# Kernel optimization log

Hardware: AMD Instinct MI355X
Metric: run time of the kernel (lower is better)

## Reference

```python
import jax, jax.numpy as jnp
import numpy as np

EMBED_DIM = 768
NUM_HEADS = 12
HEAD_DIM = EMBED_DIM // NUM_HEADS
SEGMENT_LENGTHS = [2048, 4096, 8192]
DILATION_RATES = [1, 2, 4]
SCALE = 1.0 / np.sqrt(HEAD_DIM)
B, S = 1, 8192


def setup_inputs() -> dict:
    key = jax.random.key(0)
    ks = jax.random.split(key, 5)
    std = 1.0 / np.sqrt(EMBED_DIM)
    return {
        "x": jax.random.normal(ks[0], (B, S, EMBED_DIM), dtype=jnp.float32),
        "Wqkv": jax.random.normal(ks[1], (EMBED_DIM, 3 * EMBED_DIM), dtype=jnp.float32) * std,
        "bqkv": jax.random.normal(ks[2], (3 * EMBED_DIM,), dtype=jnp.float32) * 0.01,
        "Wout": jax.random.normal(ks[3], (EMBED_DIM, EMBED_DIM), dtype=jnp.float32) * std,
        "bout": jax.random.normal(ks[4], (EMBED_DIM,), dtype=jnp.float32) * 0.01,
    }


def _attend(q, k, v):
    # q,k,v: [B,H,L,D]; full softmax attention (non-causal)
    scores = jnp.einsum("bhqd,bhkd->bhqk", q, k) * SCALE
    w = jax.nn.softmax(scores, axis=-1)
    return jnp.einsum("bhqk,bhkd->bhqd", w, v)


def reference(x, Wqkv, bqkv, Wout, bout):
    b, s, _ = x.shape
    qkv = x @ Wqkv + bqkv                                  # [B,S,3E]
    qkv = qkv.reshape(b, s, 3, NUM_HEADS, HEAD_DIM)
    qkv = jnp.transpose(qkv, (2, 0, 3, 1, 4))              # [3,B,H,S,D]
    q, k, v = qkv[0], qkv[1], qkv[2]

    outputs = []
    for seg_len, dil in zip(SEGMENT_LENGTHS, DILATION_RATES):
        if seg_len > s:
            continue
        if dil > 1:
            idx = np.arange(0, s, dil)[:seg_len]           # static indices
            seg_out = _attend(q[:, :, idx, :], k[:, :, idx, :], v[:, :, idx, :])
            full = jnp.zeros((b, NUM_HEADS, s, HEAD_DIM), dtype=seg_out.dtype)
            full = full.at[:, :, idx, :].set(seg_out)
        else:
            seg_out = _attend(q[:, :, :seg_len, :], k[:, :, :seg_len, :], v[:, :, :seg_len, :])
            pad = s - seg_out.shape[2]
            full = jnp.pad(seg_out, ((0, 0), (0, 0), (0, pad), (0, 0))) if pad > 0 else seg_out
        outputs.append(full)

    out = jnp.mean(jnp.stack(outputs), axis=0) if len(outputs) > 1 else outputs[0]
    out = jnp.transpose(out, (0, 2, 1, 3)).reshape(b, s, EMBED_DIM)
    return out @ Wout + bout
```

## Files before the change

### kernel.cpp

```cpp
#include <hip/hip_runtime.h>
#include <hip/hip_bf16.h>

typedef float f32x4 __attribute__((ext_vector_type(4)));
typedef float fvec4 __attribute__((ext_vector_type(4)));
typedef __bf16 bf16x8 __attribute__((ext_vector_type(8)));
typedef __bf16 bf16x2 __attribute__((ext_vector_type(2)));

__device__ inline float fexp2(float x) {
#if __has_builtin(__builtin_amdgcn_exp2f)
    return __builtin_amdgcn_exp2f(x);
#else
    return exp2f(x);
#endif
}

__device__ __forceinline__ bf16x2 pk_bf16(float a, float b) {
#if __has_builtin(__builtin_amdgcn_cvt_pk_bf16_f32)
    auto t = __builtin_amdgcn_cvt_pk_bf16_f32(a, b);
    return __builtin_bit_cast(bf16x2, t);
#else
    bf16x2 r; r[0] = (__bf16)a; r[1] = (__bf16)b; return r;
#endif
}

#define MFMA_BF16(a, b, c) __builtin_amdgcn_mfma_f32_16x16x32_bf16((a), (b), (c), 0, 0, 0)
#define SCHED_FENCE() __builtin_amdgcn_sched_barrier(0)

__device__ __forceinline__ void gl2lds16(const void* g, void* l) {
    __builtin_amdgcn_global_load_lds((const __attribute__((address_space(1))) void*)g,
                                     (__attribute__((address_space(3))) void*)l, 16, 0, 0);
}

#define SEG1OFF ((size_t)12 * 2048 * 64)
#define SEG2OFF ((size_t)12 * 6144 * 64)
#define QSCALE 0.18033688f

__global__ __launch_bounds__(256) void prep_kernel(
    const float* __restrict__ x, const float* __restrict__ Wqkv,
    const float* __restrict__ Wout, __bf16* __restrict__ xb,
    __bf16* __restrict__ WqkvT, __bf16* __restrict__ WoutT) {
    int bid = blockIdx.x, tid = threadIdx.x;
    if (bid < 3072) {
        int i = bid * 256 + tid;
        fvec4 a = ((const fvec4*)x)[2 * i];
        fvec4 b = ((const fvec4*)x)[2 * i + 1];
        bf16x8 o;
        o[0] = (__bf16)a[0]; o[1] = (__bf16)a[1]; o[2] = (__bf16)a[2]; o[3] = (__bf16)a[3];
        o[4] = (__bf16)b[0]; o[5] = (__bf16)b[1]; o[6] = (__bf16)b[2]; o[7] = (__bf16)b[3];
        ((bf16x8*)xb)[i] = o;
    } else if (bid < 3936) {
        int b = bid - 3072;
        int n = (b % 9) * 256 + tid;
        int kg = b / 9;
        bf16x8 o;
#pragma unroll
        for (int j = 0; j < 8; j++) o[j] = (__bf16)Wqkv[(size_t)(kg * 8 + j) * 2304 + n];
        *(bf16x8*)&WqkvT[(size_t)n * 768 + kg * 8] = o;
    } else {
        int b = bid - 3936;
        int n = (b % 3) * 256 + tid;
        int kg = b / 3;
        bf16x8 o;
#pragma unroll
        for (int j = 0; j < 8; j++) o[j] = (__bf16)Wout[(size_t)(kg * 8 + j) * 768 + n];
        *(bf16x8*)&WoutT[(size_t)n * 768 + kg * 8] = o;
    }
}

__global__ __launch_bounds__(256) void vtrans_kernel(const __bf16* __restrict__ Vc,
                                                     __bf16* __restrict__ Vt) {
    __shared__ __bf16 T[64][68];
    int bid = blockIdx.x;
    int Lc, head, t;
    size_t soff;
    if (bid < 768)       { Lc = 4096; head = bid >> 6; t = bid & 63; soff = SEG1OFF; }
    else if (bid < 1152) { int i = bid - 768; Lc = 2048; head = i >> 5; t = i & 31; soff = 0; }
    else                 { int i = bid - 1152; Lc = 2048; head = i >> 5; t = i & 31; soff = SEG2OFF; }
    const __bf16* src = Vc + soff + (size_t)head * Lc * 64;
    __bf16* dst = Vt + soff + (size_t)head * 64 * Lc;
    int tid = threadIdx.x;
#pragma unroll
    for (int it = 0; it < 2; it++) {
        int s = tid + it * 256;
        int kvr = s >> 3, d8 = (s & 7) * 8;
        bf16x8 vv = *(const bf16x8*)&src[(size_t)(t * 64 + kvr) * 64 + d8];
#pragma unroll
        for (int j = 0; j < 8; j++) T[d8 + j][kvr] = vv[j];
    }
    __syncthreads();
#pragma unroll
    for (int it = 0; it < 2; it++) {
        int s = tid + it * 256;
        int d = s >> 3, ck = s & 7;
        int kb = (ck >> 2) * 32 + (ck & 3) * 4;
        bf16x8 o;
#pragma unroll
        for (int J = 0; J < 8; J++) o[J] = T[d][kb + (J & 3) + (J >> 2) * 16];
        *(bf16x8*)&dst[(size_t)d * Lc + t * 64 + ck * 8] = o;
    }
}

__global__ __launch_bounds__(256, 2) void gemm_qkv_kernel(
    const __bf16* __restrict__ Ab, const __bf16* __restrict__ Bt,
    const float* __restrict__ bias,
    __bf16* __restrict__ Qc, __bf16* __restrict__ Kc, __bf16* __restrict__ Vc) {
    __shared__ __align__(16) char smem[65536];
    __bf16* T = (__bf16*)smem;
    int tid = threadIdx.x;
    int wave = tid >> 6, lane = tid & 63;
    int quad = lane >> 4, l15 = lane & 15;
    int bm = blockIdx.x * 128, bn = blockIdx.y * 128;
    int wm = (wave >> 1) * 64, wn = (wave & 1) * 64;
    int swzA = tid & 7;
    int rows_[4], chs_[4];
#pragma unroll
    for (int j = 0; j < 4; j++) {
        int s = j * 256 + tid;
        rows_[j] = s >> 3;
        chs_[j] = swzA ^ (rows_[j] & 7);
    }
    f32x4 acc[4][4] = {};
    {
#pragma unroll
        for (int j = 0; j < 4; j++) {
            gl2lds16(&Ab[(size_t)(bm + rows_[j]) * 768 + chs_[j] * 8],
                     smem + j * 4096 + wave * 1024);
            gl2lds16(&Bt[(size_t)(bn + rows_[j]) * 768 + chs_[j] * 8],
                     smem + 16384 + j * 4096 + wave * 1024);
        }
    }
    for (int ki = 0; ki < 12; ki++) {
        __syncthreads();
        int cur = ki & 1;
        if (ki + 1 < 12) {
            int nb = (cur ^ 1) * 32768;
            int k1 = (ki + 1) * 64;
#pragma unroll
            for (int j = 0; j < 4; j++) {
                gl2lds16(&Ab[(size_t)(bm + rows_[j]) * 768 + k1 + chs_[j] * 8],
                         smem + nb + j * 4096 + wave * 1024);
                gl2lds16(&Bt[(size_t)(bn + rows_[j]) * 768 + k1 + chs_[j] * 8],
                         smem + nb + 16384 + j * 4096 + wave * 1024);
            }
        }
        const __bf16* Al = (const __bf16*)(smem + cur * 32768);
        const __bf16* Bl = Al + 8192;
#pragma unroll
        for (int ks = 0; ks < 2; ks++) {
            bf16x8 af[4], bfr[4];
#pragma unroll
            for (int i = 0; i < 4; i++) {
                int row = wm + i * 16 + l15;
                af[i] = *(const bf16x8*)&Al[row * 64 + (((ks * 4 + quad) ^ (row & 7)) * 8)];
            }
#pragma unroll
            for (int j = 0; j < 4; j++) {
                int row = wn + j * 16 + l15;
                bfr[j] = *(const bf16x8*)&Bl[row * 64 + (((ks * 4 + quad) ^ (row & 7)) * 8)];
            }
#pragma unroll
            for (int i = 0; i < 4; i++)
#pragma unroll
                for (int j = 0; j < 4; j++)
                    acc[i][j] = MFMA_BF16(af[i], bfr[j], acc[i][j]);
        }
    }
    int which = blockIdx.y / 6;
    int h0 = (blockIdx.y % 6) * 2;
    float scl = which == 0 ? QSCALE : 1.0f;
    float bv[4];
#pragma unroll
    for (int j = 0; j < 4; j++) bv[j] = bias[bn + wn + j * 16 + l15];
    __syncthreads();
#pragma unroll
    for (int i = 0; i < 4; i++)
#pragma unroll
        for (int j = 0; j < 4; j++) {
            int col = wn + j * 16 + l15;
#pragma unroll
            for (int r = 0; r < 4; r++) {
                int row = wm + i * 16 + quad * 4 + r;
                int ch = ((col >> 3) & 8) | (((col >> 3) & 7) ^ (row & 7));
                T[row * 136 + ch * 8 + (col & 7)] =
                    (__bf16)((acc[i][j][r] + bv[j]) * scl);
            }
        }
    __syncthreads();
    __bf16* dst = which == 0 ? Qc : (which == 1 ? Kc : Vc);
    int rr = tid >> 4;
    int c8 = tid & 15;
    int hh = c8 >> 3, d8 = c8 & 7;
    int h = h0 + hh;
    __bf16* p0 = dst + ((size_t)h * 2048 * 64) + d8 * 8;
    __bf16* p1 = dst + SEG1OFF + ((size_t)h * 4096 * 64) + d8 * 8;
    __bf16* p2 = dst + SEG2OFF + ((size_t)h * 2048 * 64) + d8 * 8;
#pragma unroll
    for (int pass = 0; pass < 8; pass++) {
        int row = pass * 16 + rr;
        int pos = bm + row;
        int ch = (c8 & 8) | ((c8 & 7) ^ (row & 7));
        bf16x8 v = *(const bf16x8*)&T[row * 136 + ch * 8];
        if (pos < 2048) *(bf16x8*)&p0[(size_t)pos * 64] = v;
        if (!(pos & 1)) *(bf16x8*)&p1[(size_t)(pos >> 1) * 64] = v;
        if (!(pos & 3)) *(bf16x8*)&p2[(size_t)(pos >> 2) * 64] = v;
    }
}

__global__ __launch_bounds__(256) void gemm_out_kernel(
    const __bf16* __restrict__ Ab, const __bf16* __restrict__ Bt,
    const float* __restrict__ bias, float* __restrict__ Co) {
    __shared__ __align__(16) char smem[49152];
    int tid = threadIdx.x;
    int wave = tid >> 6, lane = tid & 63;
    int quad = lane >> 4, l15 = lane & 15;
    int bm = blockIdx.x * 64, bn = blockIdx.y * 128;
    int wn = wave * 32;
    int rowsA[2], chsA[2], rowsB[4], chsB[4];
#pragma unroll
    for (int j = 0; j < 2; j++) {
        int s = j * 256 + tid;
        rowsA[j] = s >> 3;
        chsA[j] = (s & 7) ^ (rowsA[j] & 7);
    }
#pragma unroll
    for (int j = 0; j < 4; j++) {
        int s = j * 256 + tid;
        rowsB[j] = s >> 3;
        chsB[j] = (s & 7) ^ (rowsB[j] & 7);
    }
    f32x4 acc[4][2] = {};
    {
#pragma unroll
        for (int j = 0; j < 2; j++)
            gl2lds16(&Ab[(size_t)(bm + rowsA[j]) * 768 + chsA[j] * 8],
                     smem + j * 4096 + wave * 1024);
#pragma unroll
        for (int j = 0; j < 4; j++)
            gl2lds16(&Bt[(size_t)(bn + rowsB[j]) * 768 + chsB[j] * 8],
                     smem + 8192 + j * 4096 + wave * 1024);
    }
    for (int ki = 0; ki < 12; ki++) {
        __syncthreads();
        int cur = ki & 1;
        if (ki + 1 < 12) {
            int nb = (cur ^ 1) * 24576;
            int k1 = (ki + 1) * 64;
#pragma unroll
            for (int j = 0; j < 2; j++)
                gl2lds16(&Ab[(size_t)(bm + rowsA[j]) * 768 + k1 + chsA[j] * 8],
                         smem + nb + j * 4096 + wave * 1024);
#pragma unroll
            for (int j = 0; j < 4; j++)
                gl2lds16(&Bt[(size_t)(bn + rowsB[j]) * 768 + k1 + chsB[j] * 8],
                         smem + nb + 8192 + j * 4096 + wave * 1024);
        }
        const __bf16* Al = (const __bf16*)(smem + cur * 24576);
        const __bf16* Bl = Al + 4096;
#pragma unroll
        for (int ks = 0; ks < 2; ks++) {
            bf16x8 af[4], bfr[2];
#pragma unroll
            for (int i = 0; i < 4; i++) {
                int row = i * 16 + l15;
                af[i] = *(const bf16x8*)&Al[row * 64 + (((ks * 4 + quad) ^ (row & 7)) * 8)];
            }
#pragma unroll
            for (int j = 0; j < 2; j++) {
                int row = wn + j * 16 + l15;
                bfr[j] = *(const bf16x8*)&Bl[row * 64 + (((ks * 4 + quad) ^ (row & 7)) * 8)];
            }
#pragma unroll
            for (int i = 0; i < 4; i++)
#pragma unroll
                for (int j = 0; j < 2; j++)
                    acc[i][j] = MFMA_BF16(af[i], bfr[j], acc[i][j]);
        }
    }
#pragma unroll
    for (int j = 0; j < 2; j++) {
        int c = bn + wn + j * 16 + l15;
        float bv = bias[c];
#pragma unroll
        for (int i = 0; i < 4; i++)
#pragma unroll
            for (int r = 0; r < 4; r++) {
                int row = bm + i * 16 + quad * 4 + r;
                Co[(size_t)row * 768 + c] = acc[i][j][r] + bv;
            }
    }
}

__global__ __launch_bounds__(256, 2) void attn_kernel(
    const __bf16* __restrict__ Qcb, const __bf16* __restrict__ Kcb,
    const __bf16* __restrict__ Vtb,
    float* __restrict__ O0, float* __restrict__ O1a, float* __restrict__ O1b,
    float* __restrict__ O1c, float* __restrict__ O1d, float* __restrict__ O2,
    float* __restrict__ L0, float* __restrict__ L1a, float* __restrict__ L1b,
    float* __restrict__ L1c, float* __restrict__ L1d, float* __restrict__ L2) {
    __shared__ __bf16 Kl[2 * 4096];
    __shared__ __bf16 Vl[2 * 4096];
    int bid = blockIdx.x;
    int seg, piece = 0, head, qt, Lc, iters;
    if (bid < 192)      { seg = 0; head = bid >> 4; qt = bid & 15; Lc = 2048; iters = 32; }
    else if (bid < 384) { int i = bid - 192; seg = 2; head = i >> 4; qt = i & 15; Lc = 2048; iters = 32; }
    else                { int i = bid - 384; seg = 1; head = i >> 7; int r = i & 127;
                          qt = r >> 2; piece = r & 3; Lc = 4096; iters = 16; }
    size_t soff = seg == 0 ? 0 : (seg == 1 ? SEG1OFF : SEG2OFF);
    const __bf16* Qh = Qcb + soff + (size_t)head * Lc * 64;
    const __bf16* Kh = Kcb + soff + (size_t)head * Lc * 64;
    const __bf16* Vh = Vtb + soff + (size_t)head * 64 * Lc;
    float* Ob;
    float* Lb;
    if (seg == 0)      { Ob = O0; Lb = L0 + head * 2048; }
    else if (seg == 2) { Ob = O2; Lb = L2 + head * 2048; }
    else {
        Ob = piece == 0 ? O1a : (piece == 1 ? O1b : (piece == 2 ? O1c : O1d));
        Lb = (piece == 0 ? L1a : (piece == 1 ? L1b : (piece == 2 ? L1c : L1d))) + head * 4096;
    }
    int kvb = piece * 16;
    int tid = threadIdx.x, wave = tid >> 6, lane = tid & 63;
    int quad = lane >> 4, l15 = lane & 15;
    bf16x8 qf[2][2];
#pragma unroll
    for (int qg = 0; qg < 2; qg++) {
        size_t qpos = (size_t)(qt * 128 + wave * 32 + qg * 16 + l15);
        qf[qg][0] = *(const bf16x8*)&Qh[qpos * 64 + quad * 8];
        qf[qg][1] = *(const bf16x8*)&Qh[qpos * 64 + 32 + quad * 8];
    }
    f32x4 o[2][4] = {};
    f32x4 lacc[2] = {};
    bf16x8 ones;
#pragma unroll
    for (int j = 0; j < 8; j++) ones[j] = (__bf16)1.0f;
    int kv0 = tid >> 3, cl0 = tid & 7;
    int kdb0 = cl0 ^ (kv0 & 7);
    int kv1 = kv0 + 32, kdb1 = cl0 ^ (kv1 & 7);
    char* KlB = (char*)Kl;
    char* VlB = (char*)Vl;
    int swz = l15 & 7;
    {
        int t0 = kvb * 64;
        gl2lds16(&Kh[(size_t)(t0 + kv0) * 64 + kdb0 * 8], KlB + wave * 1024);
        gl2lds16(&Kh[(size_t)(t0 + kv1) * 64 + kdb1 * 8], KlB + 4096 + wave * 1024);
        SCHED_FENCE();
        gl2lds16(&Vh[(size_t)kv0 * Lc + t0 + kdb0 * 8], VlB + wave * 1024);
        gl2lds16(&Vh[(size_t)kv1 * Lc + t0 + kdb1 * 8], VlB + 4096 + wave * 1024);
    }
    for (int nt = 0; nt < iters; nt++) {
        int cur = nt & 1;
        SCHED_FENCE();
        asm volatile("s_waitcnt vmcnt(2)" ::: "memory");
        __builtin_amdgcn_s_barrier();
        SCHED_FENCE();
        if (nt + 1 < iters) {
            int nb = 8192 * (cur ^ 1);
            int t1 = (kvb + nt + 1) * 64;
            gl2lds16(&Kh[(size_t)(t1 + kv0) * 64 + kdb0 * 8], KlB + nb + wave * 1024);
            gl2lds16(&Kh[(size_t)(t1 + kv1) * 64 + kdb1 * 8], KlB + nb + 4096 + wave * 1024);
            SCHED_FENCE();
            gl2lds16(&Vh[(size_t)kv0 * Lc + t1 + kdb0 * 8], VlB + nb + wave * 1024);
            gl2lds16(&Vh[(size_t)kv1 * Lc + t1 + kdb1 * 8], VlB + nb + 4096 + wave * 1024);
        }
        SCHED_FENCE();
        const __bf16* Kt = Kl + cur * 4096;
        const __bf16* Vt_ = Vl + cur * 4096;
        f32x4 sarr[4][2];
        __builtin_amdgcn_s_setprio(1);
#pragma unroll
        for (int c = 0; c < 4; c++) {
            int krow = (c * 16 + l15) * 64;
            bf16x8 kf0 = *(const bf16x8*)&Kt[krow + ((quad ^ swz) * 8)];
            bf16x8 kf1 = *(const bf16x8*)&Kt[krow + (((4 + quad) ^ swz) * 8)];
#pragma unroll
            for (int qg = 0; qg < 2; qg++) {
                f32x4 z = {};
                z = MFMA_BF16(kf0, qf[qg][0], z);
                sarr[c][qg] = MFMA_BF16(kf1, qf[qg][1], z);
            }
        }
        __builtin_amdgcn_s_setprio(0);
        union { bf16x8 v8; bf16x2 v2[4]; } pf8[2][2];
#pragma unroll
        for (int qg = 0; qg < 2; qg++)
#pragma unroll
            for (int c = 0; c < 4; c++) {
                float p0 = fexp2(sarr[c][qg][0]);
                float p1 = fexp2(sarr[c][qg][1]);
                float p2 = fexp2(sarr[c][qg][2]);
                float p3 = fexp2(sarr[c][qg][3]);
                pf8[qg][c >> 1].v2[(c & 1) * 2 + 0] = pk_bf16(p0, p1);
                pf8[qg][c >> 1].v2[(c & 1) * 2 + 1] = pk_bf16(p2, p3);
            }
        SCHED_FENCE();
        if (nt + 1 < iters) {
            asm volatile("s_waitcnt vmcnt(4)" ::: "memory");
        } else {
            asm volatile("s_waitcnt vmcnt(0)" ::: "memory");
        }
        __builtin_amdgcn_s_barrier();
        SCHED_FENCE();
        __builtin_amdgcn_s_setprio(1);
#pragma unroll
        for (int u = 0; u < 2; u++) {
#pragma unroll
            for (int ds = 0; ds < 4; ds++) {
                int d = ds * 16 + l15;
                bf16x8 vf = *(const bf16x8*)&Vt_[d * 64 + (((u * 4 + quad) ^ swz) * 8)];
                o[0][ds] = MFMA_BF16(vf, pf8[0][u].v8, o[0][ds]);
                o[1][ds] = MFMA_BF16(vf, pf8[1][u].v8, o[1][ds]);
            }
            lacc[0] = MFMA_BF16(ones, pf8[0][u].v8, lacc[0]);
            lacc[1] = MFMA_BF16(ones, pf8[1][u].v8, lacc[1]);
        }
        __builtin_amdgcn_s_setprio(0);
    }
#pragma unroll
    for (int qg = 0; qg < 2; qg++) {
        float l = lacc[qg][0];
        int pos = qt * 128 + wave * 32 + qg * 16 + l15;
        float* orow = Ob + (size_t)pos * 768 + head * 64;
#pragma unroll
        for (int ds = 0; ds < 4; ds++)
            *(f32x4*)&orow[ds * 16 + quad * 4] = o[qg][ds];
        if (lane < 16) Lb[qt * 128 + wave * 32 + qg * 16 + lane] = l;
    }
}

__global__ __launch_bounds__(256) void combine_kernel(
    const float* __restrict__ O0, const float* __restrict__ O1a,
    const float* __restrict__ O1b, const float* __restrict__ O1c,
    const float* __restrict__ O1d, const float* __restrict__ O2,
    const float* __restrict__ L0, const float* __restrict__ L1a,
    const float* __restrict__ L1b, const float* __restrict__ L1c,
    const float* __restrict__ L1d, const float* __restrict__ L2,
    __bf16* __restrict__ attnF) {
    int g = blockIdx.x * 256 + threadIdx.x;
    int q = g / 96;
    int cs = (g - q * 96) * 8;
    int head = cs >> 6;
    f32x4 a0 = {}, a1 = {};
    if (q < 2048) {
        float inv = 1.0f / L0[head * 2048 + q];
        const f32x4* p = (const f32x4*)&O0[(size_t)q * 768 + cs];
        a0 += p[0] * inv; a1 += p[1] * inv;
    }
    if (!(q & 1)) {
        int p1 = q >> 1;
        int li = head * 4096 + p1;
        float inv = 1.0f / (L1a[li] + L1b[li] + L1c[li] + L1d[li]);
        size_t ro = (size_t)p1 * 768 + cs;
        const f32x4* pa = (const f32x4*)&O1a[ro];
        const f32x4* pb = (const f32x4*)&O1b[ro];
        const f32x4* pc = (const f32x4*)&O1c[ro];
        const f32x4* pd = (const f32x4*)&O1d[ro];
        a0 += ((pa[0] + pb[0]) + (pc[0] + pd[0])) * inv;
        a1 += ((pa[1] + pb[1]) + (pc[1] + pd[1])) * inv;
    }
    if (!(q & 3)) {
        int p2 = q >> 2;
        float inv = 1.0f / L2[head * 2048 + p2];
        const f32x4* p = (const f32x4*)&O2[(size_t)p2 * 768 + cs];
        a0 += p[0] * inv; a1 += p[1] * inv;
    }
    const float third = 1.0f / 3.0f;
    bf16x8 ov;
    ov[0] = (__bf16)(a0[0] * third); ov[1] = (__bf16)(a0[1] * third);
    ov[2] = (__bf16)(a0[2] * third); ov[3] = (__bf16)(a0[3] * third);
    ov[4] = (__bf16)(a1[0] * third); ov[5] = (__bf16)(a1[1] * third);
    ov[6] = (__bf16)(a1[2] * third); ov[7] = (__bf16)(a1[3] * third);
    *(bf16x8*)&attnF[(size_t)q * 768 + cs] = ov;
}

extern "C" void kernel_launch(void* const* d_in, const int* in_sizes, int n_in,
                              void* d_out, int out_size, void* d_ws, size_t ws_size,
                              hipStream_t stream) {
    const float* x    = (const float*)d_in[0];
    const float* Wqkv = (const float*)d_in[1];
    const float* bqkv = (const float*)d_in[2];
    const float* Wout = (const float*)d_in[3];
    const float* bout = (const float*)d_in[4];
    float* out = (float*)d_out;
    (void)in_sizes; (void)n_in; (void)out_size; (void)ws_size;

    char* ws = (char*)d_ws;
    size_t off = 0;
    auto take = [&](size_t bytes) -> void* {
        void* p = ws + off;
        off += (bytes + 255) & ~(size_t)255;
        return p;
    };
    const size_t QKV_ELEMS = (size_t)12 * 8192 * 64;
    __bf16* xb    = (__bf16*)take((size_t)8192 * 768 * 2);
    __bf16* WqkvT = (__bf16*)take((size_t)2304 * 768 * 2);
    __bf16* WoutT = (__bf16*)take((size_t)768 * 768 * 2);
    __bf16* Qc    = (__bf16*)take(QKV_ELEMS * 2);
    __bf16* Kc    = (__bf16*)take(QKV_ELEMS * 2);
    __bf16* Vc    = (__bf16*)take(QKV_ELEMS * 2);
    __bf16* Vt    = (__bf16*)take(QKV_ELEMS * 2);
    float*  O1a   = (float*)take((size_t)4096 * 768 * 4);
    float*  O1b   = (float*)take((size_t)4096 * 768 * 4);
    float*  O1c   = (float*)take((size_t)4096 * 768 * 4);
    float*  L0    = (float*)take((size_t)12 * 2048 * 4);
    float*  L1a   = (float*)take((size_t)12 * 4096 * 4);
    float*  L1b   = (float*)take((size_t)12 * 4096 * 4);
    float*  L1c   = (float*)take((size_t)12 * 4096 * 4);
    float*  L1d   = (float*)take((size_t)12 * 4096 * 4);
    float*  L2    = (float*)take((size_t)12 * 2048 * 4);
    float*  O0    = (float*)xb;
    float*  O2    = O0 + (size_t)2048 * 768;
    float*  O1d   = (float*)Vc;
    __bf16* attnF = Qc;

    prep_kernel<<<4224, 256, 0, stream>>>(x, Wqkv, Wout, xb, WqkvT, WoutT);
    gemm_qkv_kernel<<<dim3(64, 18), 256, 0, stream>>>(xb, WqkvT, bqkv, Qc, Kc, Vc);
    vtrans_kernel<<<1536, 256, 0, stream>>>(Vc, Vt);
    attn_kernel<<<1920, 256, 0, stream>>>(Qc, Kc, Vt, O0, O1a, O1b, O1c, O1d, O2,
                                          L0, L1a, L1b, L1c, L1d, L2);
    combine_kernel<<<3072, 256, 0, stream>>>(O0, O1a, O1b, O1c, O1d, O2,
                                             L0, L1a, L1b, L1c, L1d, L2, attnF);
    gemm_out_kernel<<<dim3(128, 6), 256, 0, stream>>>(attnF, WoutT, bout, out);
}
```

Measured before the change: 244.7 us.

## Fuse V transpose into QKV GEMM epilogue and reorder attention block mapping

Removes the separate V-transpose kernel. The QKV GEMM epilogue now writes V directly in transposed, permuted layout for all three dilated segments, reading from the swizzled shared-memory tile. This saves a kernel launch and a round trip of V through global memory, at the cost of strided shared-memory gathers in the epilogue. Separately, the attention kernel's block index mapping now places the head innermost, which changes the order in which blocks are scheduled and may affect cache locality.

```diff
diff --git a/kernel.cpp b/kernel.cpp
--- a/kernel.cpp
+++ b/kernel.cpp
@@ -67,43 +67,10 @@
     }
 }
 
-__global__ __launch_bounds__(256) void vtrans_kernel(const __bf16* __restrict__ Vc,
-                                                     __bf16* __restrict__ Vt) {
-    __shared__ __bf16 T[64][68];
-    int bid = blockIdx.x;
-    int Lc, head, t;
-    size_t soff;
-    if (bid < 768)       { Lc = 4096; head = bid >> 6; t = bid & 63; soff = SEG1OFF; }
-    else if (bid < 1152) { int i = bid - 768; Lc = 2048; head = i >> 5; t = i & 31; soff = 0; }
-    else                 { int i = bid - 1152; Lc = 2048; head = i >> 5; t = i & 31; soff = SEG2OFF; }
-    const __bf16* src = Vc + soff + (size_t)head * Lc * 64;
-    __bf16* dst = Vt + soff + (size_t)head * 64 * Lc;
-    int tid = threadIdx.x;
-#pragma unroll
-    for (int it = 0; it < 2; it++) {
-        int s = tid + it * 256;
-        int kvr = s >> 3, d8 = (s & 7) * 8;
-        bf16x8 vv = *(const bf16x8*)&src[(size_t)(t * 64 + kvr) * 64 + d8];
-#pragma unroll
-        for (int j = 0; j < 8; j++) T[d8 + j][kvr] = vv[j];
-    }
-    __syncthreads();
-#pragma unroll
-    for (int it = 0; it < 2; it++) {
-        int s = tid + it * 256;
-        int d = s >> 3, ck = s & 7;
-        int kb = (ck >> 2) * 32 + (ck & 3) * 4;
-        bf16x8 o;
-#pragma unroll
-        for (int J = 0; J < 8; J++) o[J] = T[d][kb + (J & 3) + (J >> 2) * 16];
-        *(bf16x8*)&dst[(size_t)d * Lc + t * 64 + ck * 8] = o;
-    }
-}
-
 __global__ __launch_bounds__(256, 2) void gemm_qkv_kernel(
     const __bf16* __restrict__ Ab, const __bf16* __restrict__ Bt,
     const float* __restrict__ bias,
-    __bf16* __restrict__ Qc, __bf16* __restrict__ Kc, __bf16* __restrict__ Vc) {
+    __bf16* __restrict__ Qc, __bf16* __restrict__ Kc, __bf16* __restrict__ Vt) {
     __shared__ __align__(16) char smem[65536];
     __bf16* T = (__bf16*)smem;
     int tid = threadIdx.x;
@@ -186,23 +153,89 @@
             }
         }
     __syncthreads();
-    __bf16* dst = which == 0 ? Qc : (which == 1 ? Kc : Vc);
-    int rr = tid >> 4;
-    int c8 = tid & 15;
-    int hh = c8 >> 3, d8 = c8 & 7;
-    int h = h0 + hh;
-    __bf16* p0 = dst + ((size_t)h * 2048 * 64) + d8 * 8;
-    __bf16* p1 = dst + SEG1OFF + ((size_t)h * 4096 * 64) + d8 * 8;
-    __bf16* p2 = dst + SEG2OFF + ((size_t)h * 2048 * 64) + d8 * 8;
-#pragma unroll
-    for (int pass = 0; pass < 8; pass++) {
-        int row = pass * 16 + rr;
-        int pos = bm + row;
-        int ch = (c8 & 8) | ((c8 & 7) ^ (row & 7));
-        bf16x8 v = *(const bf16x8*)&T[row * 136 + ch * 8];
-        if (pos < 2048) *(bf16x8*)&p0[(size_t)pos * 64] = v;
-        if (!(pos & 1)) *(bf16x8*)&p1[(size_t)(pos >> 1) * 64] = v;
-        if (!(pos & 3)) *(bf16x8*)&p2[(size_t)(pos >> 2) * 64] = v;
+    if (which < 2) {
+        __bf16* dst = which == 0 ? Qc : Kc;
+        int rr = tid >> 4;
+        int c8 = tid & 15;
+        int hh = c8 >> 3, d8 = c8 & 7;
+        int h = h0 + hh;
+        __bf16* p0 = dst + ((size_t)h * 2048 * 64) + d8 * 8;
+        __bf16* p1 = dst + SEG1OFF + ((size_t)h * 4096 * 64) + d8 * 8;
+        __bf16* p2 = dst + SEG2OFF + ((size_t)h * 2048 * 64) + d8 * 8;
+#pragma unroll
+        for (int pass = 0; pass < 8; pass++) {
+            int row = pass * 16 + rr;
+            int pos = bm + row;
+            int ch = (c8 & 8) | ((c8 & 7) ^ (row & 7));
+            bf16x8 v = *(const bf16x8*)&T[row * 136 + ch * 8];
+            if (pos < 2048) *(bf16x8*)&p0[(size_t)pos * 64] = v;
+            if (!(pos & 1)) *(bf16x8*)&p1[(size_t)(pos >> 1) * 64] = v;
+            if (!(pos & 3)) *(bf16x8*)&p2[(size_t)(pos >> 2) * 64] = v;
+        }
+    } else {
+        {
+            __bf16* base1 = Vt + SEG1OFF;
+#pragma unroll
+            for (int it = 0; it < 4; it++) {
+                int sid = it * 256 + tid;
+                int hh = sid >> 9, ck = (sid >> 6) & 7, d = sid & 63;
+                int col = hh * 64 + d;
+                int kb = (ck >> 2) * 32 + (ck & 3) * 4;
+                bf16x8 o;
+#pragma unroll
+                for (int J = 0; J < 8; J++) {
+                    int k = kb + (J & 3) + (J >> 2) * 16;
+                    int r = 2 * k;
+                    int sc = ((col >> 3) & 8) | (((col >> 3) & 7) ^ (r & 7));
+                    o[J] = T[r * 136 + sc * 8 + (col & 7)];
+                }
+                *(bf16x8*)&base1[(size_t)(h0 + hh) * 64 * 4096 + (size_t)d * 4096 +
+                                 (bm >> 1) + ck * 8] = o;
+            }
+        }
+        if (bm < 2048) {
+#pragma unroll
+            for (int it = 0; it < 8; it++) {
+                int sid = it * 256 + tid;
+                int tsub = sid >> 10, rest = sid & 1023;
+                int hh = rest >> 9, ck = (rest >> 6) & 7, d = rest & 63;
+                int col = hh * 64 + d;
+                int kb = (ck >> 2) * 32 + (ck & 3) * 4;
+                bf16x8 o;
+#pragma unroll
+                for (int J = 0; J < 8; J++) {
+                    int k = kb + (J & 3) + (J >> 2) * 16;
+                    int r = tsub * 64 + k;
+                    int sc = ((col >> 3) & 8) | (((col >> 3) & 7) ^ (r & 7));
+                    o[J] = T[r * 136 + sc * 8 + (col & 7)];
+                }
+                *(bf16x8*)&Vt[(size_t)(h0 + hh) * 64 * 2048 + (size_t)d * 2048 +
+                              bm + tsub * 64 + ck * 8] = o;
+            }
+        }
+        {
+            __bf16* base2 = Vt + SEG2OFF;
+            int ckoff = (bm & 128) ? 4 : 0;
+            int rsub = (bm & 128) ? 128 : 0;
+#pragma unroll
+            for (int it = 0; it < 2; it++) {
+                int sid = it * 256 + tid;
+                int hh = sid >> 8, cki = (sid >> 6) & 3, d = sid & 63;
+                int ck = cki + ckoff;
+                int col = hh * 64 + d;
+                int kb = (ck >> 2) * 32 + (ck & 3) * 4;
+                bf16x8 o;
+#pragma unroll
+                for (int J = 0; J < 8; J++) {
+                    int k = kb + (J & 3) + (J >> 2) * 16;
+                    int r = 4 * k - rsub;
+                    int sc = ((col >> 3) & 8) | (((col >> 3) & 7) ^ (r & 7));
+                    o[J] = T[r * 136 + sc * 8 + (col & 7)];
+                }
+                *(bf16x8*)&base2[(size_t)(h0 + hh) * 64 * 2048 + (size_t)d * 2048 +
+                                 (bm >> 8) * 64 + ck * 8] = o;
+            }
+        }
     }
 }
 
@@ -301,10 +334,10 @@
     __shared__ __bf16 Vl[2 * 4096];
     int bid = blockIdx.x;
     int seg, piece = 0, head, qt, Lc, iters;
-    if (bid < 192)      { seg = 0; head = bid >> 4; qt = bid & 15; Lc = 2048; iters = 32; }
-    else if (bid < 384) { int i = bid - 192; seg = 2; head = i >> 4; qt = i & 15; Lc = 2048; iters = 32; }
-    else                { int i = bid - 384; seg = 1; head = i >> 7; int r = i & 127;
-                          qt = r >> 2; piece = r & 3; Lc = 4096; iters = 16; }
+    if (bid < 192)      { seg = 0; head = bid % 12; qt = bid / 12; Lc = 2048; iters = 32; }
+    else if (bid < 384) { int i = bid - 192; seg = 2; head = i % 12; qt = i / 12; Lc = 2048; iters = 32; }
+    else                { int i = bid - 384; seg = 1; head = i % 12; int rest = i / 12;
+                          qt = rest >> 2; piece = rest & 3; Lc = 4096; iters = 16; }
     size_t soff = seg == 0 ? 0 : (seg == 1 ? SEG1OFF : SEG2OFF);
     const __bf16* Qh = Qcb + soff + (size_t)head * Lc * 64;
     const __bf16* Kh = Kcb + soff + (size_t)head * Lc * 64;
@@ -512,8 +545,7 @@
     __bf16* attnF = Qc;
 
     prep_kernel<<<4224, 256, 0, stream>>>(x, Wqkv, Wout, xb, WqkvT, WoutT);
-    gemm_qkv_kernel<<<dim3(64, 18), 256, 0, stream>>>(xb, WqkvT, bqkv, Qc, Kc, Vc);
-    vtrans_kernel<<<1536, 256, 0, stream>>>(Vc, Vt);
+    gemm_qkv_kernel<<<dim3(64, 18), 256, 0, stream>>>(xb, WqkvT, bqkv, Qc, Kc, Vt);
     attn_kernel<<<1920, 256, 0, stream>>>(Qc, Kc, Vt, O0, O1a, O1b, O1c, O1d, O2,
                                           L0, L1a, L1b, L1c, L1d, L2);
     combine_kernel<<<3072, 256, 0, stream>>>(O0, O1a, O1b, O1c, O1d, O2,
```

Result: no change. 243.4 us (-0.5%).
